# Kernel optimization log

Hardware: AMD Instinct MI355X
Metric: run time of the kernel (lower is better)

The kernel has to match this reference:

```python
import math
import jax, jax.numpy as jnp
import numpy as np

FACIL_RATE = 2.0
FIRE_THRESH = 0.85
MAX_GATE = 8.0
EPS = 1e-12  # F.normalize eps

B, T, D = 8, 4096, 2048


def _gelu(x):
    # tanh-approx GELU, exactly as in the torch module
    c = math.sqrt(2.0 / math.pi)
    return 0.5 * x * (1.0 + jnp.tanh(c * (x + 0.044715 * x * x * x)))


def _l2norm(v, axis=-1):
    n = jnp.sqrt(jnp.sum(v * v, axis=axis, keepdims=True))
    return v / jnp.maximum(n, EPS)


def setup_inputs() -> dict:
    key = jax.random.key(0)
    k1, k2 = jax.random.split(key)
    x = jax.random.normal(k1, (B, T, D), dtype=jnp.float32)
    pos_buf = jax.random.normal(k2, (T, D), dtype=jnp.float32)
    pos_facil = jnp.ones((T,), dtype=jnp.float32)
    log_k_pos = jnp.asarray(math.log(0.5), dtype=jnp.float32)
    return {"x": x, "log_k_pos": log_k_pos, "pos_buf": pos_buf, "pos_facil": pos_facil}


def reference(x, log_k_pos, pos_buf, pos_facil):
    # steady-state (pass1 complete) path of GELU275.forward
    k_pos = jnp.clip(jnp.exp(log_k_pos), 0.01, 5.0)
    y = _gelu(x)                                   # [B,T,D]
    # everything below the gelu except the final gate multiply runs under
    # no_grad / on y.detach() in torch -> stop_gradient here
    y_det = jax.lax.stop_gradient(y)
    pos_buf_n = _l2norm(jax.lax.stop_gradient(pos_buf))          # [T,D]
    y_n = _l2norm(y_det)                                          # [B,T,D]
    sim = jnp.einsum("btd,td->bt", y_n, pos_buf_n)               # cosine sim [B,T]
    fire_mask = jnp.mean(sim, axis=0) > FIRE_THRESH              # [T]
    pf = jax.lax.stop_gradient(pos_facil)
    facil_t = jnp.where(fire_mask, jnp.minimum(pf * FACIL_RATE, 16.0), pf)  # [T]
    gate = jnp.minimum(1.0 + k_pos * (facil_t[None, :] - 1.0) * sim, MAX_GATE)  # [B,T]
    return y * gate[:, :, None]
```

## Files before the change

### kernel.cpp

```cpp
#include <hip/hip_runtime.h>
#include <math.h>

#define BB 8
#define TT 4096
#define DD 2048
#define THREADS 512
#define NT 8
#define NBLK (TT / NT)
#define SMEM_BYTES ((2 * (BB * DD + DD)) * 4)

typedef float v4f __attribute__((ext_vector_type(4)));

__device__ __forceinline__ float gelu_fast(float x) {
    const float c1 = 1.5957691216057308f;
    const float c2 = 0.07135481282556483f;
    float e = __expf(-x * fmaf(c2, x * x, c1));
    return x * __builtin_amdgcn_rcpf(1.0f + e);
}

__device__ __forceinline__ void gl2lds(const float* g, float* l) {
    __builtin_amdgcn_global_load_lds(
        (const __attribute__((address_space(1))) void*)g,
        (__attribute__((address_space(3))) void*)l, 16, 0, 0);
}

__global__ __launch_bounds__(THREADS, 2) void gelu275_fused(
    const float* __restrict__ x,
    const float* __restrict__ log_k_pos,
    const float* __restrict__ pos_buf,
    const float* __restrict__ pos_facil,
    float* __restrict__ out)
{
    extern __shared__ __align__(16) float smem[];
    float* const xbuf0 = smem;
    float* const xbuf1 = smem + BB * DD;
    float* const pbuf0 = smem + 2 * BB * DD;
    float* const pbuf1 = pbuf0 + DD;
    __shared__ float s_red[2][17];

    const int tid  = threadIdx.x;
    const int lane = tid & 63;
    const int wave = tid >> 6;
    const int t0   = blockIdx.x * NT;
    const int base = lane * 4;

    const float kp = fminf(fmaxf(__expf(log_k_pos[0]), 0.01f), 5.0f);
    float pfv[NT];
#pragma unroll
    for (int i = 0; i < NT; ++i) pfv[i] = pos_facil[t0 + i];

    {
        const float* xrow = x + ((size_t)wave * TT + t0) * DD;
#pragma unroll
        for (int c = 0; c < 8; ++c)
            gl2lds(xrow + c * 256 + base, xbuf0 + wave * DD + c * 256);
        gl2lds(pos_buf + (size_t)t0 * DD + wave * 256 + base,
               pbuf0 + wave * 256);
    }

#pragma unroll
    for (int i = 0; i < NT; ++i) {
        float* const xb = (i & 1) ? xbuf1 : xbuf0;
        float* const pb = (i & 1) ? pbuf1 : pbuf0;

        if (i == 0) { asm volatile("s_waitcnt vmcnt(0)" ::: "memory"); }
        else        { asm volatile("s_waitcnt vmcnt(8)" ::: "memory"); }
        __builtin_amdgcn_s_barrier();
        asm volatile("" ::: "memory");

        if (i + 1 < NT) {
            float* const xn = (i & 1) ? xbuf0 : xbuf1;
            float* const pn = (i & 1) ? pbuf0 : pbuf1;
            const float* xrow = x + ((size_t)wave * TT + (t0 + i + 1)) * DD;
#pragma unroll
            for (int c = 0; c < 8; ++c)
                gl2lds(xrow + c * 256 + base, xn + wave * DD + c * 256);
            gl2lds(pos_buf + (size_t)(t0 + i + 1) * DD + wave * 256 + base,
                   pn + wave * 256);
        }

        v4f Y[8];
        float dot = 0.f, yn2 = 0.f, pn2 = 0.f;
#pragma unroll
        for (int c = 0; c < 8; ++c) {
            v4f v       = *(const v4f*)(xb + wave * DD + c * 256 + base);
            const v4f p = *(const v4f*)(pb + c * 256 + base);
            v.x = gelu_fast(v.x); v.y = gelu_fast(v.y);
            v.z = gelu_fast(v.z); v.w = gelu_fast(v.w);
            Y[c] = v;
            dot += v.x * p.x + v.y * p.y + v.z * p.z + v.w * p.w;
            yn2 += v.x * v.x + v.y * v.y + v.z * v.z + v.w * v.w;
            pn2 += p.x * p.x + p.y * p.y + p.z * p.z + p.w * p.w;
        }

#pragma unroll
        for (int off = 32; off; off >>= 1) {
            dot += __shfl_xor(dot, off);
            yn2 += __shfl_xor(yn2, off);
            pn2 += __shfl_xor(pn2, off);
        }
        if (lane == 0) {
            s_red[i & 1][wave]     = dot;
            s_red[i & 1][8 + wave] = yn2;
            if (wave == 0) s_red[i & 1][16] = pn2;
        }
        asm volatile("s_waitcnt lgkmcnt(0)" ::: "memory");
        __builtin_amdgcn_s_barrier();
        asm volatile("" ::: "memory");

        const float pnn = fmaxf(sqrtf(s_red[i & 1][16]), 1e-12f);
        float simsum = 0.f, simw = 0.f;
#pragma unroll
        for (int bb = 0; bb < BB; ++bb) {
            const float s = s_red[i & 1][bb] *
                __builtin_amdgcn_rcpf(
                    fmaxf(sqrtf(s_red[i & 1][8 + bb]), 1e-12f) * pnn);
            simsum += s;
            if (bb == wave) simw = s;
        }
        const bool  fire  = (simsum * 0.125f) > 0.85f;
        const float pf    = pfv[i];
        const float facil = fire ? fminf(pf * 2.0f, 16.0f) : pf;
        const float g     = fminf(1.0f + kp * (facil - 1.0f) * simw, 8.0f);

        float* orow = out + ((size_t)wave * TT + (t0 + i)) * DD + base;
#pragma unroll
        for (int c = 0; c < 8; ++c) {
            v4f o = Y[c];
            o.x *= g; o.y *= g; o.z *= g; o.w *= g;
            *(v4f*)(orow + c * 256) = o;
        }
    }
}

extern "C" void kernel_launch(void* const* d_in, const int* in_sizes, int n_in,
                              void* d_out, int out_size, void* d_ws, size_t ws_size,
                              hipStream_t stream) {
    const float* x          = (const float*)d_in[0];
    const float* log_k_pos  = (const float*)d_in[1];
    const float* pos_buf    = (const float*)d_in[2];
    const float* pos_facil  = (const float*)d_in[3];
    float* out              = (float*)d_out;

    (void)hipFuncSetAttribute((const void*)gelu275_fused,
                              hipFuncAttributeMaxDynamicSharedMemorySize,
                              SMEM_BYTES);

    dim3 grid(NBLK);
    dim3 block(THREADS);
    gelu275_fused<<<grid, block, SMEM_BYTES, stream>>>(
        x, log_k_pos, pos_buf, pos_facil, out);
}
```

Before: 120.7 us.

## Split each row into half-row stages to halve LDS and raise occupancy

Each timestep row is now streamed in two half-row stages through the double buffer, which halves the LDS footprint so launch bounds can request four blocks per CU instead of two. The pos_buf half-rows are loaded with 4-byte global-to-LDS loads, and the vmcnt waits are retuned for the new mix of outstanding loads. The aim is more resident waves to hide HBM latency on this memory-bound kernel. The cost is a barrier per half-row, partial-sum state kept across stages, and many narrow loads that raise instruction count. Register pressure under the tighter launch bound could also cause spills.

```diff
diff --git a/kernel.cpp b/kernel.cpp
--- a/kernel.cpp
+++ b/kernel.cpp
@@ -4,10 +4,12 @@
 #define BB 8
 #define TT 4096
 #define DD 2048
+#define HALF 1024
 #define THREADS 512
 #define NT 8
 #define NBLK (TT / NT)
-#define SMEM_BYTES ((2 * (BB * DD + DD)) * 4)
+#define NG (NT * 2)
+#define SMEM_BYTES ((2 * BB * HALF + 2 * HALF) * 4)
 
 typedef float v4f __attribute__((ext_vector_type(4)));
 
@@ -18,13 +20,18 @@
     return x * __builtin_amdgcn_rcpf(1.0f + e);
 }
 
-__device__ __forceinline__ void gl2lds(const float* g, float* l) {
+__device__ __forceinline__ void gl2lds16(const float* g, float* l) {
     __builtin_amdgcn_global_load_lds(
         (const __attribute__((address_space(1))) void*)g,
         (__attribute__((address_space(3))) void*)l, 16, 0, 0);
 }
+__device__ __forceinline__ void gl2lds4(const float* g, float* l) {
+    __builtin_amdgcn_global_load_lds(
+        (const __attribute__((address_space(1))) void*)g,
+        (__attribute__((address_space(3))) void*)l, 4, 0, 0);
+}
 
-__global__ __launch_bounds__(THREADS, 2) void gelu275_fused(
+__global__ __launch_bounds__(THREADS, 4) void gelu275_fused(
     const float* __restrict__ x,
     const float* __restrict__ log_k_pos,
     const float* __restrict__ pos_buf,
@@ -33,10 +40,10 @@
 {
     extern __shared__ __align__(16) float smem[];
     float* const xbuf0 = smem;
-    float* const xbuf1 = smem + BB * DD;
-    float* const pbuf0 = smem + 2 * BB * DD;
-    float* const pbuf1 = pbuf0 + DD;
-    __shared__ float s_red[2][17];
+    float* const xbuf1 = smem + BB * HALF;
+    float* const pbuf0 = smem + 2 * BB * HALF;
+    float* const pbuf1 = pbuf0 + HALF;
+    __shared__ float s_red[17];
 
     const int tid  = threadIdx.x;
     const int lane = tid & 63;
@@ -49,86 +56,103 @@
 #pragma unroll
     for (int i = 0; i < NT; ++i) pfv[i] = pos_facil[t0 + i];
 
+    const float* xrow = x       + ((size_t)wave * TT + t0) * DD;
+    const float* prow = pos_buf + (size_t)t0 * DD;
+    float*       orow = out     + ((size_t)wave * TT + t0) * DD;
+
     {
-        const float* xrow = x + ((size_t)wave * TT + t0) * DD;
 #pragma unroll
-        for (int c = 0; c < 8; ++c)
-            gl2lds(xrow + c * 256 + base, xbuf0 + wave * DD + c * 256);
-        gl2lds(pos_buf + (size_t)t0 * DD + wave * 256 + base,
-               pbuf0 + wave * 256);
+        for (int c = 0; c < 4; ++c)
+            gl2lds16(xrow + c * 256 + base, xbuf0 + wave * HALF + c * 256);
+        gl2lds4(prow + wave * 128 + lane,      pbuf0 + wave * 128);
+        gl2lds4(prow + wave * 128 + 64 + lane, pbuf0 + wave * 128 + 64);
     }
 
+    v4f Y[8];
+    float dot = 0.f, yn2 = 0.f, pn2 = 0.f;
+
 #pragma unroll
-    for (int i = 0; i < NT; ++i) {
-        float* const xb = (i & 1) ? xbuf1 : xbuf0;
-        float* const pb = (i & 1) ? pbuf1 : pbuf0;
+    for (int g = 0; g < NG; ++g) {
+        const int tloc = g >> 1;
+        const int h    = g & 1;
+        float* const xc = h ? xbuf1 : xbuf0;
+        float* const pc = h ? pbuf1 : pbuf0;
 
-        if (i == 0) { asm volatile("s_waitcnt vmcnt(0)" ::: "memory"); }
-        else        { asm volatile("s_waitcnt vmcnt(8)" ::: "memory"); }
+        if (g + 1 < NG) {
+            const int tn = (g + 1) >> 1;
+            const int hn = (g + 1) & 1;
+            float* const xn = hn ? xbuf1 : xbuf0;
+            float* const pn = hn ? pbuf1 : pbuf0;
+            const float* xs = xrow + (size_t)tn * DD + hn * HALF;
+            const float* pp = prow + (size_t)tn * DD + hn * HALF;
+#pragma unroll
+            for (int c = 0; c < 4; ++c)
+                gl2lds16(xs + c * 256 + base, xn + wave * HALF + c * 256);
+            gl2lds4(pp + wave * 128 + lane,      pn + wave * 128);
+            gl2lds4(pp + wave * 128 + 64 + lane, pn + wave * 128 + 64);
+        }
+
+        if (g == 0)           { asm volatile("s_waitcnt vmcnt(6)"  ::: "memory"); }
+        else if (g == NG - 1) { asm volatile("s_waitcnt vmcnt(0)"  ::: "memory"); }
+        else if (h == 0)      { asm volatile("s_waitcnt vmcnt(14)" ::: "memory"); }
+        else                  { asm volatile("s_waitcnt vmcnt(6)"  ::: "memory"); }
         __builtin_amdgcn_s_barrier();
         asm volatile("" ::: "memory");
 
-        if (i + 1 < NT) {
-            float* const xn = (i & 1) ? xbuf0 : xbuf1;
-            float* const pn = (i & 1) ? pbuf0 : pbuf1;
-            const float* xrow = x + ((size_t)wave * TT + (t0 + i + 1)) * DD;
+        if (h == 0) { dot = 0.f; yn2 = 0.f; pn2 = 0.f; }
 #pragma unroll
-            for (int c = 0; c < 8; ++c)
-                gl2lds(xrow + c * 256 + base, xn + wave * DD + c * 256);
-            gl2lds(pos_buf + (size_t)(t0 + i + 1) * DD + wave * 256 + base,
-                   pn + wave * 256);
-        }
-
-        v4f Y[8];
-        float dot = 0.f, yn2 = 0.f, pn2 = 0.f;
-#pragma unroll
-        for (int c = 0; c < 8; ++c) {
-            v4f v       = *(const v4f*)(xb + wave * DD + c * 256 + base);
-            const v4f p = *(const v4f*)(pb + c * 256 + base);
+        for (int c = 0; c < 4; ++c) {
+            v4f v       = *(const v4f*)(xc + wave * HALF + c * 256 + base);
+            const v4f p = *(const v4f*)(pc + c * 256 + base);
             v.x = gelu_fast(v.x); v.y = gelu_fast(v.y);
             v.z = gelu_fast(v.z); v.w = gelu_fast(v.w);
-            Y[c] = v;
+            Y[h * 4 + c] = v;
             dot += v.x * p.x + v.y * p.y + v.z * p.z + v.w * p.w;
             yn2 += v.x * v.x + v.y * v.y + v.z * v.z + v.w * v.w;
             pn2 += p.x * p.x + p.y * p.y + p.z * p.z + p.w * p.w;
         }
 
+        if (h == 1) {
 #pragma unroll
-        for (int off = 32; off; off >>= 1) {
-            dot += __shfl_xor(dot, off);
-            yn2 += __shfl_xor(yn2, off);
-            pn2 += __shfl_xor(pn2, off);
+            for (int off = 32; off; off >>= 1) {
+                dot += __shfl_xor(dot, off);
+                yn2 += __shfl_xor(yn2, off);
+                pn2 += __shfl_xor(pn2, off);
+            }
+            if (lane == 0) {
+                s_red[wave]     = dot;
+                s_red[8 + wave] = yn2;
+                if (wave == 0) s_red[16] = pn2;
+            }
         }
-        if (lane == 0) {
-            s_red[i & 1][wave]     = dot;
-            s_red[i & 1][8 + wave] = yn2;
-            if (wave == 0) s_red[i & 1][16] = pn2;
-        }
+
         asm volatile("s_waitcnt lgkmcnt(0)" ::: "memory");
         __builtin_amdgcn_s_barrier();
         asm volatile("" ::: "memory");
 
-        const float pnn = fmaxf(sqrtf(s_red[i & 1][16]), 1e-12f);
-        float simsum = 0.f, simw = 0.f;
+        if (h == 1) {
+            const float pnn = fmaxf(sqrtf(s_red[16]), 1e-12f);
+            float simsum = 0.f, simw = 0.f;
 #pragma unroll
-        for (int bb = 0; bb < BB; ++bb) {
-            const float s = s_red[i & 1][bb] *
-                __builtin_amdgcn_rcpf(
-                    fmaxf(sqrtf(s_red[i & 1][8 + bb]), 1e-12f) * pnn);
-            simsum += s;
-            if (bb == wave) simw = s;
-        }
-        const bool  fire  = (simsum * 0.125f) > 0.85f;
-        const float pf    = pfv[i];
-        const float facil = fire ? fminf(pf * 2.0f, 16.0f) : pf;
-        const float g     = fminf(1.0f + kp * (facil - 1.0f) * simw, 8.0f);
+            for (int bb = 0; bb < BB; ++bb) {
+                const float s = s_red[bb] *
+                    __builtin_amdgcn_rcpf(
+                        fmaxf(sqrtf(s_red[8 + bb]), 1e-12f) * pnn);
+                simsum += s;
+                if (bb == wave) simw = s;
+            }
+            const bool  fire  = (simsum * 0.125f) > 0.85f;
+            const float pf    = pfv[tloc];
+            const float facil = fire ? fminf(pf * 2.0f, 16.0f) : pf;
+            const float gt    = fminf(1.0f + kp * (facil - 1.0f) * simw, 8.0f);
 
-        float* orow = out + ((size_t)wave * TT + (t0 + i)) * DD + base;
+            float* o = orow + (size_t)tloc * DD;
 #pragma unroll
-        for (int c = 0; c < 8; ++c) {
-            v4f o = Y[c];
-            o.x *= g; o.y *= g; o.z *= g; o.w *= g;
-            *(v4f*)(orow + c * 256) = o;
+            for (int k = 0; k < 8; ++k) {
+                v4f ov = Y[k];
+                ov.x *= gt; ov.y *= gt; ov.z *= gt; ov.w *= gt;
+                *(v4f*)(o + (k >> 2) * HALF + (k & 3) * 256 + base) = ov;
+            }
         }
     }
 }
```

New measurement: 120.6 us (median of 2 runs). Within noise of the previous version (-0.1%).
